# Optimization experiments

Hardware: AMD Instinct MI355X
Metric: run time of the kernel (lower is better)

Reference implementation:

```python
import jax, jax.numpy as jnp
import numpy as np

SELECT_SIZE = 64
SM_SCALE = 0.07216878364870322  # 192 ** -0.5
V_HEAD_DIM = 128


def setup_inputs() -> dict:
    key = jax.random.key(0)
    k1, k2, k3, k4 = jax.random.split(key, 4)
    B, S, Hq, G, TOPK = 4, 2048, 16, 4, 16
    T = B * S
    NB = S // SELECT_SIZE  # 32 blocks per sequence
    q = jax.random.normal(k1, (T, Hq, 192), dtype=jnp.float32)
    k = jax.random.normal(k2, (T, Hq, 192), dtype=jnp.float32)
    v = jax.random.normal(k3, (T, Hq, V_HEAD_DIM), dtype=jnp.float32)
    idx = jax.random.randint(k4, (T, G, TOPK), 0, NB, dtype=jnp.int32)
    # guarantee block 0 is always selected so every causal row has >=1 valid key
    idx = idx.at[..., 0].set(0)
    idx = jnp.sort(idx, axis=-1)
    return {"q": q, "k": k, "v": v, "selected_indices": idx,
            "batch_size": B, "seq_len": S}


def reference(q, k, v, selected_indices, batch_size, seq_len):
    B, S = batch_size, seq_len
    Hq = q.shape[1]
    G = selected_indices.shape[1]
    Hg = Hq // G  # query heads per selection-score group
    nb = (S + SELECT_SIZE - 1) // SELECT_SIZE
    dv = v.shape[-1]

    # un-ragged: B equal-length sequences
    qg = q.reshape(B, S, G, Hg, -1)
    kg = k.reshape(B, S, G, Hg, -1)
    vg = v.reshape(B, S, G, Hg, -1)
    idx = selected_indices.reshape(B, S, G, -1)

    # which KV blocks are selected for each (query position, group): [B,S,G,nb]
    allowed_blk = (idx[..., None] == jnp.arange(nb, dtype=idx.dtype)).any(axis=-2)
    blk_of_pos = jnp.arange(S) // SELECT_SIZE
    pos_ok = allowed_blk[..., blk_of_pos]  # [B, Tq, G, Skv]
    causal = jnp.arange(S)[:, None] >= jnp.arange(S)[None, :]
    mask = pos_ok & causal[None, :, None, :]          # [B, Tq, G, Skv]
    mask = mask.transpose(0, 2, 1, 3)[:, :, None]      # [B, G, 1, Tq, Skv]

    scores = jnp.einsum('btghd,bsghd->bghts', qg, kg) * SM_SCALE
    scores = jnp.where(mask, scores, jnp.float32(-1e30))
    attn = jax.nn.softmax(scores, axis=-1)
    o = jnp.einsum('bghts,bsghd->btghd', attn, vg)
    return o.reshape(B * S, Hq * dv)
```

## Files before the change

### kernel.cpp

```cpp
#include <hip/hip_runtime.h>


typedef __attribute__((ext_vector_type(8))) _Float16 half8;
typedef __attribute__((ext_vector_type(4))) float f32x4;

__device__ __forceinline__ half8 cvt8(const float4* p) {
  float4 a = p[0], b = p[1];
  half8 r;
  r[0] = (_Float16)a.x; r[1] = (_Float16)a.y; r[2] = (_Float16)a.z; r[3] = (_Float16)a.w;
  r[4] = (_Float16)b.x; r[5] = (_Float16)b.y; r[6] = (_Float16)b.z; r[7] = (_Float16)b.w;
  return r;
}

__device__ __forceinline__ half8 cvt8s(const float4* p, float s) {
  float4 a = p[0], b = p[1];
  half8 r;
  r[0] = (_Float16)(a.x * s); r[1] = (_Float16)(a.y * s);
  r[2] = (_Float16)(a.z * s); r[3] = (_Float16)(a.w * s);
  r[4] = (_Float16)(b.x * s); r[5] = (_Float16)(b.y * s);
  r[6] = (_Float16)(b.z * s); r[7] = (_Float16)(b.w * s);
  return r;
}

__device__ __forceinline__ void async16(const void* g, void* l) {
  __builtin_amdgcn_global_load_lds(
      (const __attribute__((address_space(1))) void*)g,
      (__attribute__((address_space(3))) void*)l, 16, 0, 0);
}

template <int CTRL>
__device__ __forceinline__ float dpp_mov(float x) {
  union { float f; int i; } u;
  u.f = x;
  u.i = __builtin_amdgcn_update_dpp(u.i, u.i, CTRL, 0xf, 0xf, true);
  return u.f;
}
__device__ __forceinline__ float row16_max(float r) {
  r = fmaxf(r, dpp_mov<0xB1>(r));
  r = fmaxf(r, dpp_mov<0x4E>(r));
  r = fmaxf(r, dpp_mov<0x141>(r));
  r = fmaxf(r, dpp_mov<0x140>(r));
  return r;
}
__device__ __forceinline__ float row16_sum(float r) {
  r += dpp_mov<0xB1>(r);
  r += dpp_mov<0x4E>(r);
  r += dpp_mov<0x141>(r);
  r += dpp_mov<0x140>(r);
  return r;
}

__global__ __launch_bounds__(256) void kv_prep(const float* __restrict__ k,
                                               const float* __restrict__ v,
                                               _Float16* __restrict__ kf,
                                               _Float16* __restrict__ vf) {
  __shared__ float lb[64 * 196];
  int blk = blockIdx.x;
  int bh = blk >> 5, kb = blk & 31;
  int b = bh >> 4, h = bh & 15;
  int tid = threadIdx.x;

  const float* ksrc = k + ((long)(b * 2048 + kb * 64) * 16 + h) * 192;
#pragma unroll
  for (int it = 0; it < 12; ++it) {
    int idx = it * 256 + tid;
    int kk = idx / 48, c4 = idx - kk * 48;
    *(float4*)(&lb[kk * 196 + c4 * 4]) = *(const float4*)(ksrc + (long)kk * 3072 + c4 * 4);
  }
  __syncthreads();
  _Float16* kdst = kf + (long)blk * 12288;
#pragma unroll
  for (int it = 0; it < 6; ++it) {
    int oct = it * 256 + tid;
    int frag = oct >> 6, lane = oct & 63;
    int ntile = frag / 6, kc = frag - ntile * 6;
    int n = ntile * 16 + (lane & 15);
    int d = kc * 32 + ((lane >> 4) << 3);
    *(half8*)(kdst + (long)oct * 8) = cvt8((const float4*)(&lb[n * 196 + d]));
  }
  __syncthreads();

  const float* vsrc = v + ((long)(b * 2048 + kb * 64) * 16 + h) * 128;
#pragma unroll
  for (int it = 0; it < 8; ++it) {
    int idx = it * 256 + tid;
    int kk = idx >> 5, c4 = idx & 31;
    *(float4*)(&lb[kk * 132 + c4 * 4]) = *(const float4*)(vsrc + (long)kk * 2048 + c4 * 4);
  }
  __syncthreads();
  _Float16* vdst = vf + (long)blk * 8192;
#pragma unroll
  for (int it = 0; it < 4; ++it) {
    int oct = it * 256 + tid;
    int frag = oct >> 6, lane = oct & 63;
    int n0 = frag >> 1, kc = frag & 1;
    int dv = n0 * 16 + (lane & 15);
    int kbase = kc * 32 + ((lane >> 4) << 3);
    half8 o;
#pragma unroll
    for (int j = 0; j < 8; ++j) o[j] = (_Float16)lb[(kbase + j) * 132 + dv];
    *(half8*)(vdst + (long)oct * 8) = o;
  }
}

__global__ __launch_bounds__(256) void attn_main(const float* __restrict__ q,
                                                 const int* __restrict__ idx,
                                                 const _Float16* __restrict__ kf,
                                                 const _Float16* __restrict__ vf,
                                                 float* __restrict__ out) {
  constexpr float SCL = 0.07216878364870322f * 1.4426950408889634f;
  int id = (int)blockIdx.x;
  int qb = 31 - (id >> 6);
  int h = id & 15, b = (id >> 4) & 3, g = h >> 2;
  int tid = threadIdx.x;
  int w = tid >> 6, L = tid & 63;
  int Lm = L & 15, Lq = L >> 4;
  int m0 = w * 16;
  int t0 = b * 2048 + qb * 64;

  __shared__ __align__(16) char sh_kv[40960];
  __shared__ __align__(16) _Float16 Pbuf[4][16 * 72];
  __shared__ unsigned un_sh[4];
  char* lk = sh_kv;
  char* lv = sh_kv + 24576;

  half8 qa[6];
  const float* qrow = q + ((long)(t0 + m0 + Lm) * 16 + h) * 192;
#pragma unroll
  for (int c = 0; c < 6; ++c) qa[c] = cvt8s((const float4*)(qrow + c * 32 + Lq * 8), SCL);

  unsigned mrow = 0;
  {
    const int* ip = idx + ((long)(t0 + m0 + Lm) * 4 + g) * 16;
#pragma unroll
    for (int j = 0; j < 16; ++j) mrow |= (1u << ip[j]);
  }
  unsigned un = mrow;
#pragma unroll
  for (int o = 32; o; o >>= 1) un |= __shfl_xor(un, o, 64);
  unsigned smask[4];
#pragma unroll
  for (int i = 0; i < 4; ++i) smask[i] = __shfl(mrow, Lq * 4 + i, 64);
  if (L == 0) un_sh[w] = un;
  __syncthreads();
  unsigned bm = un_sh[0] | un_sh[1] | un_sh[2] | un_sh[3];

  f32x4 Oacc[8];
#pragma unroll
  for (int n0 = 0; n0 < 8; ++n0) Oacc[n0] = (f32x4){0.f, 0.f, 0.f, 0.f};
  float m_i[4] = {-1e30f, -1e30f, -1e30f, -1e30f};
  float l_i[4] = {0.f, 0.f, 0.f, 0.f};

  const char* kfb = (const char*)(kf + (long)((b * 16 + h) * 32) * 12288);
  const char* vfb = (const char*)(vf + (long)((b * 16 + h) * 32) * 8192);
  _Float16* pw = &Pbuf[w][0];
  const half8* lkf = (const half8*)lk;
  const half8* lvf = (const half8*)lv;

  auto stage = [&](int kb) {
    const char* kg = kfb + (long)kb * 24576;
    const char* vg = vfb + (long)kb * 16384;
#pragma unroll
    for (int c = 0; c < 6; ++c) {
      int ch = w + c * 4;
      async16(kg + ch * 1024 + L * 16, lk + ch * 1024);
    }
#pragma unroll
    for (int c = 0; c < 4; ++c) {
      int ch = w + c * 4;
      async16(vg + ch * 1024 + L * 16, lv + ch * 1024);
    }
  };

  auto compute = [&](int kb, bool lastb) __attribute__((always_inline)) {
    f32x4 S[4];
#pragma unroll
    for (int nt = 0; nt < 4; ++nt) {
      f32x4 acc = {0.f, 0.f, 0.f, 0.f};
#pragma unroll
      for (int c = 0; c < 6; ++c)
        acc = __builtin_amdgcn_mfma_f32_16x16x32_f16(qa[c], lkf[(nt * 6 + c) * 64 + L], acc, 0, 0, 0);
      S[nt] = acc;
    }

    _Float16 pf[4][4];
    if (!lastb) {
      float msel[4];
#pragma unroll
      for (int i = 0; i < 4; ++i) msel[i] = ((smask[i] >> kb) & 1u) ? 1.0f : 0.0f;
      float rmax[4] = {-1e30f, -1e30f, -1e30f, -1e30f};
#pragma unroll
      for (int nt = 0; nt < 4; ++nt)
#pragma unroll
        for (int i = 0; i < 4; ++i) rmax[i] = fmaxf(rmax[i], S[nt][i]);
#pragma unroll
      for (int i = 0; i < 4; ++i) rmax[i] = row16_max(rmax[i]);
      bool up = (rmax[0] > m_i[0]) | (rmax[1] > m_i[1]) |
                (rmax[2] > m_i[2]) | (rmax[3] > m_i[3]);
      if (__any(up)) {
        f32x4 av;
#pragma unroll
        for (int i = 0; i < 4; ++i) {
          float mn = fmaxf(m_i[i], rmax[i]);
          av[i] = __builtin_amdgcn_exp2f(m_i[i] - mn);
          m_i[i] = mn;
          l_i[i] *= av[i];
        }
#pragma unroll
        for (int n0 = 0; n0 < 8; ++n0) Oacc[n0] *= av;
      }
      float psum[4] = {0.f, 0.f, 0.f, 0.f};
#pragma unroll
      for (int nt = 0; nt < 4; ++nt)
#pragma unroll
        for (int i = 0; i < 4; ++i) {
          float p = __builtin_amdgcn_exp2f(S[nt][i] - m_i[i]) * msel[i];
          pf[nt][i] = (_Float16)p;
          psum[i] += p;
        }
#pragma unroll
      for (int i = 0; i < 4; ++i) l_i[i] += row16_sum(psum[i]);
    } else {
      float rmax[4] = {-1e30f, -1e30f, -1e30f, -1e30f};
      float sc[4][4];
#pragma unroll
      for (int nt = 0; nt < 4; ++nt) {
        int key = nt * 16 + Lm;
#pragma unroll
        for (int i = 0; i < 4; ++i) {
          bool ok = ((smask[i] >> kb) & 1u) && (key <= m0 + Lq * 4 + i);
          float val = ok ? S[nt][i] : -1e30f;
          sc[nt][i] = val;
          rmax[i] = fmaxf(rmax[i], val);
        }
      }
      f32x4 av;
      float psum[4];
#pragma unroll
      for (int i = 0; i < 4; ++i) {
        float r = row16_max(rmax[i]);
        float mn = fmaxf(m_i[i], r);
        av[i] = __builtin_amdgcn_exp2f(m_i[i] - mn);
        m_i[i] = mn;
        float s = 0.f;
#pragma unroll
        for (int nt = 0; nt < 4; ++nt) {
          float p = __builtin_amdgcn_exp2f(sc[nt][i] - mn);
          pf[nt][i] = (_Float16)p;
          s += p;
        }
        psum[i] = s;
      }
#pragma unroll
      for (int i = 0; i < 4; ++i) l_i[i] = l_i[i] * av[i] + row16_sum(psum[i]);
#pragma unroll
      for (int n0 = 0; n0 < 8; ++n0) Oacc[n0] *= av;
    }

    asm volatile("s_waitcnt lgkmcnt(0)" ::: "memory");
#pragma unroll
    for (int nt = 0; nt < 4; ++nt)
#pragma unroll
      for (int i = 0; i < 4; ++i)
        pw[(Lq * 4 + i) * 72 + nt * 16 + Lm] = pf[nt][i];
    asm volatile("s_waitcnt lgkmcnt(0)" ::: "memory");

#pragma unroll
    for (int kc = 0; kc < 2; ++kc) {
      half8 afr = *(const half8*)(pw + Lm * 72 + kc * 32 + Lq * 8);
#pragma unroll
      for (int n0 = 0; n0 < 8; ++n0)
        Oacc[n0] = __builtin_amdgcn_mfma_f32_16x16x32_f16(afr, lvf[(n0 * 2 + kc) * 64 + L], Oacc[n0], 0, 0, 0);
    }
  };

  for (int kb = 0; kb < qb; ++kb) {
    if (!((bm >> kb) & 1u)) continue;
    stage(kb);
    asm volatile("s_waitcnt vmcnt(0)" ::: "memory");
    __syncthreads();
    if ((un >> kb) & 1u) compute(kb, false);
    __syncthreads();
  }
  if ((bm >> qb) & 1u) {
    stage(qb);
    asm volatile("s_waitcnt vmcnt(0)" ::: "memory");
    __syncthreads();
    if ((un >> qb) & 1u) compute(qb, true);
  }

#pragma unroll
  for (int i = 0; i < 4; ++i) l_i[i] = 1.f / l_i[i];
  float* orow = out + (long)(t0 + m0 + Lq * 4) * 2048 + h * 128 + Lm;
#pragma unroll
  for (int i = 0; i < 4; ++i)
#pragma unroll
    for (int n0 = 0; n0 < 8; ++n0)
      orow[(long)i * 2048 + n0 * 16] = Oacc[n0][i] * l_i[i];
}

extern "C" void kernel_launch(void* const* d_in, const int* in_sizes, int n_in,
                              void* d_out, int out_size, void* d_ws, size_t ws_size,
                              hipStream_t stream) {
  const float* q = (const float*)d_in[0];
  const float* k = (const float*)d_in[1];
  const float* v = (const float*)d_in[2];
  const int* idx = (const int*)d_in[3];
  _Float16* kf = (_Float16*)d_ws;
  _Float16* vf = kf + (size_t)2048 * 12288;
  float* out = (float*)d_out;
  kv_prep<<<2048, 256, 0, stream>>>(k, v, kf, vf);
  attn_main<<<2048, 256, 0, stream>>>(q, idx, kf, vf, out);
}
```

Measured before the change: 410.7 us.

## Transpose attention MFMAs so each lane owns one query row

After: 404.8 us. No clear change (-1.4%).

```diff
diff --git a/kernel.cpp b/kernel.cpp
--- a/kernel.cpp
+++ b/kernel.cpp
@@ -3,6 +3,7 @@
 
 typedef __attribute__((ext_vector_type(8))) _Float16 half8;
 typedef __attribute__((ext_vector_type(4))) float f32x4;
+typedef __attribute__((ext_vector_type(4))) unsigned int u32x4;
 
 __device__ __forceinline__ half8 cvt8(const float4* p) {
   float4 a = p[0], b = p[1];
@@ -28,25 +29,10 @@
       (__attribute__((address_space(3))) void*)l, 16, 0, 0);
 }
 
-template <int CTRL>
-__device__ __forceinline__ float dpp_mov(float x) {
-  union { float f; int i; } u;
-  u.f = x;
-  u.i = __builtin_amdgcn_update_dpp(u.i, u.i, CTRL, 0xf, 0xf, true);
-  return u.f;
-}
-__device__ __forceinline__ float row16_max(float r) {
-  r = fmaxf(r, dpp_mov<0xB1>(r));
-  r = fmaxf(r, dpp_mov<0x4E>(r));
-  r = fmaxf(r, dpp_mov<0x141>(r));
-  r = fmaxf(r, dpp_mov<0x140>(r));
-  return r;
-}
-__device__ __forceinline__ float row16_sum(float r) {
-  r += dpp_mov<0xB1>(r);
-  r += dpp_mov<0x4E>(r);
-  r += dpp_mov<0x141>(r);
-  r += dpp_mov<0x140>(r);
+__device__ __forceinline__ f32x4 vmax4(f32x4 a, f32x4 b) {
+  f32x4 r;
+  r[0] = fmaxf(a[0], b[0]); r[1] = fmaxf(a[1], b[1]);
+  r[2] = fmaxf(a[2], b[2]); r[3] = fmaxf(a[3], b[3]);
   return r;
 }
 
@@ -74,7 +60,8 @@
     int oct = it * 256 + tid;
     int frag = oct >> 6, lane = oct & 63;
     int ntile = frag / 6, kc = frag - ntile * 6;
-    int n = ntile * 16 + (lane & 15);
+    int lm = lane & 15;
+    int n = ((lm >> 2) << 4) + ntile * 4 + (lm & 3);
     int d = kc * 32 + ((lane >> 4) << 3);
     *(half8*)(kdst + (long)oct * 8) = cvt8((const float4*)(&lb[n * 196 + d]));
   }
@@ -138,9 +125,6 @@
   unsigned un = mrow;
 #pragma unroll
   for (int o = 32; o; o >>= 1) un |= __shfl_xor(un, o, 64);
-  unsigned smask[4];
-#pragma unroll
-  for (int i = 0; i < 4; ++i) smask[i] = __shfl(mrow, Lq * 4 + i, 64);
   if (L == 0) un_sh[w] = un;
   __syncthreads();
   unsigned bm = un_sh[0] | un_sh[1] | un_sh[2] | un_sh[3];
@@ -148,8 +132,7 @@
   f32x4 Oacc[8];
 #pragma unroll
   for (int n0 = 0; n0 < 8; ++n0) Oacc[n0] = (f32x4){0.f, 0.f, 0.f, 0.f};
-  float m_i[4] = {-1e30f, -1e30f, -1e30f, -1e30f};
-  float l_i[4] = {0.f, 0.f, 0.f, 0.f};
+  float m_i = -1e30f, l_i = 0.f;
 
   const char* kfb = (const char*)(kf + (long)((b * 16 + h) * 32) * 12288);
   const char* vfb = (const char*)(vf + (long)((b * 16 + h) * 32) * 8192);
@@ -179,98 +162,106 @@
       f32x4 acc = {0.f, 0.f, 0.f, 0.f};
 #pragma unroll
       for (int c = 0; c < 6; ++c)
-        acc = __builtin_amdgcn_mfma_f32_16x16x32_f16(qa[c], lkf[(nt * 6 + c) * 64 + L], acc, 0, 0, 0);
+        acc = __builtin_amdgcn_mfma_f32_16x16x32_f16(lkf[(nt * 6 + c) * 64 + L], qa[c], acc, 0, 0, 0);
       S[nt] = acc;
     }
 
-    _Float16 pf[4][4];
+    float p[4][4];
+    float msel = ((mrow >> kb) & 1u) ? 1.0f : 0.0f;
     if (!lastb) {
-      float msel[4];
-#pragma unroll
-      for (int i = 0; i < 4; ++i) msel[i] = ((smask[i] >> kb) & 1u) ? 1.0f : 0.0f;
-      float rmax[4] = {-1e30f, -1e30f, -1e30f, -1e30f};
-#pragma unroll
-      for (int nt = 0; nt < 4; ++nt)
-#pragma unroll
-        for (int i = 0; i < 4; ++i) rmax[i] = fmaxf(rmax[i], S[nt][i]);
-#pragma unroll
-      for (int i = 0; i < 4; ++i) rmax[i] = row16_max(rmax[i]);
-      bool up = (rmax[0] > m_i[0]) | (rmax[1] > m_i[1]) |
-                (rmax[2] > m_i[2]) | (rmax[3] > m_i[3]);
-      if (__any(up)) {
-        f32x4 av;
-#pragma unroll
-        for (int i = 0; i < 4; ++i) {
-          float mn = fmaxf(m_i[i], rmax[i]);
-          av[i] = __builtin_amdgcn_exp2f(m_i[i] - mn);
-          m_i[i] = mn;
-          l_i[i] *= av[i];
-        }
+      f32x4 t = vmax4(vmax4(S[0], S[1]), vmax4(S[2], S[3]));
+      float rmax = fmaxf(fmaxf(t[0], t[1]), fmaxf(t[2], t[3]));
+      rmax = fmaxf(rmax, __shfl_xor(rmax, 16));
+      rmax = fmaxf(rmax, __shfl_xor(rmax, 32));
+      if (__any(rmax > m_i)) {
+        float mn = fmaxf(m_i, rmax);
+        float av = __builtin_amdgcn_exp2f(m_i - mn);
+        m_i = mn;
+        l_i *= av;
 #pragma unroll
         for (int n0 = 0; n0 < 8; ++n0) Oacc[n0] *= av;
       }
-      float psum[4] = {0.f, 0.f, 0.f, 0.f};
+      float ps[4];
+#pragma unroll
+      for (int nt = 0; nt < 4; ++nt) {
+        float s0 = 0.f, s1 = 0.f;
+#pragma unroll
+        for (int i = 0; i < 4; i += 2) {
+          float a = __builtin_amdgcn_exp2f(S[nt][i] - m_i) * msel;
+          float c = __builtin_amdgcn_exp2f(S[nt][i + 1] - m_i) * msel;
+          p[nt][i] = a; p[nt][i + 1] = c;
+          s0 += a; s1 += c;
+        }
+        ps[nt] = s0 + s1;
+      }
+      float psum = (ps[0] + ps[1]) + (ps[2] + ps[3]);
+      psum += __shfl_xor(psum, 16);
+      psum += __shfl_xor(psum, 32);
+      l_i += psum;
+    } else {
+      float sc[4][4];
+      float rmax = -1e30f;
 #pragma unroll
       for (int nt = 0; nt < 4; ++nt)
 #pragma unroll
         for (int i = 0; i < 4; ++i) {
-          float p = __builtin_amdgcn_exp2f(S[nt][i] - m_i[i]) * msel[i];
-          pf[nt][i] = (_Float16)p;
-          psum[i] += p;
+          int key = Lq * 16 + nt * 4 + i;
+          bool ok = (msel != 0.f) && (key <= m0 + Lm);
+          float v = ok ? S[nt][i] : -1e30f;
+          sc[nt][i] = v;
+          rmax = fmaxf(rmax, v);
         }
-#pragma unroll
-      for (int i = 0; i < 4; ++i) l_i[i] += row16_sum(psum[i]);
-    } else {
-      float rmax[4] = {-1e30f, -1e30f, -1e30f, -1e30f};
-      float sc[4][4];
+      rmax = fmaxf(rmax, __shfl_xor(rmax, 16));
+      rmax = fmaxf(rmax, __shfl_xor(rmax, 32));
+      float mn = fmaxf(m_i, rmax);
+      float av = __builtin_amdgcn_exp2f(m_i - mn);
+      m_i = mn;
+      float ps[4];
 #pragma unroll
       for (int nt = 0; nt < 4; ++nt) {
-        int key = nt * 16 + Lm;
+        float s0 = 0.f;
 #pragma unroll
         for (int i = 0; i < 4; ++i) {
-          bool ok = ((smask[i] >> kb) & 1u) && (key <= m0 + Lq * 4 + i);
-          float val = ok ? S[nt][i] : -1e30f;
-          sc[nt][i] = val;
-          rmax[i] = fmaxf(rmax[i], val);
+          float a = __builtin_amdgcn_exp2f(sc[nt][i] - mn);
+          p[nt][i] = a;
+          s0 += a;
         }
+        ps[nt] = s0;
       }
-      f32x4 av;
-      float psum[4];
-#pragma unroll
-      for (int i = 0; i < 4; ++i) {
-        float r = row16_max(rmax[i]);
-        float mn = fmaxf(m_i[i], r);
-        av[i] = __builtin_amdgcn_exp2f(m_i[i] - mn);
-        m_i[i] = mn;
-        float s = 0.f;
-#pragma unroll
-        for (int nt = 0; nt < 4; ++nt) {
-          float p = __builtin_amdgcn_exp2f(sc[nt][i] - mn);
-          pf[nt][i] = (_Float16)p;
-          s += p;
-        }
-        psum[i] = s;
-      }
-#pragma unroll
-      for (int i = 0; i < 4; ++i) l_i[i] = l_i[i] * av[i] + row16_sum(psum[i]);
+      float psum = (ps[0] + ps[1]) + (ps[2] + ps[3]);
+      psum += __shfl_xor(psum, 16);
+      psum += __shfl_xor(psum, 32);
+      l_i = l_i * av + psum;
 #pragma unroll
       for (int n0 = 0; n0 < 8; ++n0) Oacc[n0] *= av;
     }
 
     asm volatile("s_waitcnt lgkmcnt(0)" ::: "memory");
-#pragma unroll
-    for (int nt = 0; nt < 4; ++nt)
-#pragma unroll
-      for (int i = 0; i < 4; ++i)
-        pw[(Lq * 4 + i) * 72 + nt * 16 + Lm] = pf[nt][i];
+    u32x4 w0, w1;
+    {
+      auto c00 = __builtin_amdgcn_cvt_pkrtz(p[0][0], p[0][1]);
+      auto c01 = __builtin_amdgcn_cvt_pkrtz(p[0][2], p[0][3]);
+      auto c10 = __builtin_amdgcn_cvt_pkrtz(p[1][0], p[1][1]);
+      auto c11 = __builtin_amdgcn_cvt_pkrtz(p[1][2], p[1][3]);
+      auto c20 = __builtin_amdgcn_cvt_pkrtz(p[2][0], p[2][1]);
+      auto c21 = __builtin_amdgcn_cvt_pkrtz(p[2][2], p[2][3]);
+      auto c30 = __builtin_amdgcn_cvt_pkrtz(p[3][0], p[3][1]);
+      auto c31 = __builtin_amdgcn_cvt_pkrtz(p[3][2], p[3][3]);
+      w0[0] = __builtin_bit_cast(unsigned, c00); w0[1] = __builtin_bit_cast(unsigned, c01);
+      w0[2] = __builtin_bit_cast(unsigned, c10); w0[3] = __builtin_bit_cast(unsigned, c11);
+      w1[0] = __builtin_bit_cast(unsigned, c20); w1[1] = __builtin_bit_cast(unsigned, c21);
+      w1[2] = __builtin_bit_cast(unsigned, c30); w1[3] = __builtin_bit_cast(unsigned, c31);
+    }
+    *(u32x4*)(pw + Lm * 72 + Lq * 16) = w0;
+    *(u32x4*)(pw + Lm * 72 + Lq * 16 + 8) = w1;
     asm volatile("s_waitcnt lgkmcnt(0)" ::: "memory");
 
 #pragma unroll
     for (int kc = 0; kc < 2; ++kc) {
-      half8 afr = *(const half8*)(pw + Lm * 72 + kc * 32 + Lq * 8);
+      half8 pfr = *(const half8*)(pw + Lm * 72 + kc * 32 + Lq * 8);
 #pragma unroll
       for (int n0 = 0; n0 < 8; ++n0)
-        Oacc[n0] = __builtin_amdgcn_mfma_f32_16x16x32_f16(afr, lvf[(n0 * 2 + kc) * 64 + L], Oacc[n0], 0, 0, 0);
+        Oacc[n0] = __builtin_amdgcn_mfma_f32_16x16x32_f16(lvf[(n0 * 2 + kc) * 64 + L], pfr, Oacc[n0], 0, 0, 0);
     }
   };
 
@@ -289,14 +280,13 @@
     if ((un >> qb) & 1u) compute(qb, true);
   }
 
-#pragma unroll
-  for (int i = 0; i < 4; ++i) l_i[i] = 1.f / l_i[i];
-  float* orow = out + (long)(t0 + m0 + Lq * 4) * 2048 + h * 128 + Lm;
-#pragma unroll
-  for (int i = 0; i < 4; ++i)
-#pragma unroll
-    for (int n0 = 0; n0 < 8; ++n0)
-      orow[(long)i * 2048 + n0 * 16] = Oacc[n0][i] * l_i[i];
+  float inv = 1.f / l_i;
+  float* orow = out + (long)(t0 + m0 + Lm) * 2048 + h * 128 + Lq * 4;
+#pragma unroll
+  for (int n0 = 0; n0 < 8; ++n0) {
+    f32x4 o = Oacc[n0] * inv;
+    *(f32x4*)(orow + n0 * 16) = o;
+  }
 }
 
 extern "C" void kernel_launch(void* const* d_in, const int* in_sizes, int n_in,
```
